# Kernel tuning notes

Measured on AMD Instinct MI355X. Metric: run time of the kernel, lower is better.

## Reference

```python
import jax, jax.numpy as jnp
import numpy as np

TAU = 2.0      # LIF membrane time constant
EPS = 1e-5     # BatchNorm eps
HEADS = 8
SCALE = 0.125
ALPHA = 4.0    # surrogate sigmoid sharpness

@jax.custom_vjp
def spike(x):
    return (x >= 0.0).astype(x.dtype)

def _spike_fwd(x):
    return spike(x), x

def _spike_bwd(x, g):
    s = jax.nn.sigmoid(ALPHA * x)
    return (g * ALPHA * s * (1.0 - s),)

spike.defvjp(_spike_fwd, _spike_bwd)

def lif(x_seq, v_th):
    # multi-step LIF, v_reset=0, hard reset; x_seq: [T, ...]
    def step(v, x):
        v = v + (x - v) / TAU
        s = spike(v - v_th)
        v = (1.0 - s) * v  # hard reset to 0
        return v, s
    v0 = jnp.zeros_like(x_seq[0])
    _, spikes = jax.lax.scan(step, v0, x_seq)
    return spikes

def bn(x, gamma, beta, mean, var):
    # inference-mode BatchNorm1d over channel axis; x: [T,B,C,N], params: [C]
    inv = gamma * jax.lax.rsqrt(var + EPS)
    return x * inv[:, None] + (beta - mean * inv)[:, None]

def setup_inputs() -> dict:
    key = jax.random.key(0)
    k1, k2 = jax.random.split(key)
    T, B, C, N, H = 4, 64, 512, 196, HEADS
    x = jax.random.normal(k1, (T, B, C, N), dtype=jnp.float32)
    res_attn = jnp.zeros((T, B, H, N, N), dtype=jnp.float32)
    w = jax.random.normal(k2, (4, C, C), dtype=jnp.float32) / np.sqrt(C)
    bn_gamma = jnp.ones((4, C), dtype=jnp.float32)
    bn_beta = jnp.zeros((4, C), dtype=jnp.float32)
    bn_mean = jnp.zeros((4, C), dtype=jnp.float32)
    bn_var = jnp.ones((4, C), dtype=jnp.float32)
    return {"x": x, "res_attn": res_attn, "w": w, "bn_gamma": bn_gamma,
            "bn_beta": bn_beta, "bn_mean": bn_mean, "bn_var": bn_var}

def reference(x, res_attn, w, bn_gamma, bn_beta, bn_mean, bn_var):
    T, B, C, N = x.shape
    H = HEADS
    D = C // H

    def qkv_branch(i):
        y = jnp.einsum('oc,tbcn->tbon', w[i], x)          # conv1x1
        y = bn(y, bn_gamma[i], bn_beta[i], bn_mean[i], bn_var[i])
        return lif(y, 1.0)                                # binary spikes

    def to_heads(t):  # [T,B,C,N] -> [T,B,H,N,D]
        return t.transpose(0, 1, 3, 2).reshape(T, B, N, H, D).transpose(0, 1, 3, 2, 4)

    q = to_heads(qkv_branch(0))
    k = to_heads(qkv_branch(1))
    v = to_heads(qkv_branch(2))

    attn = jnp.einsum('tbhnd,tbhmd->tbhnm', q, k) * SCALE
    o = jnp.einsum('tbhnm,tbhmd->tbhnd', attn, v)
    o = o.transpose(0, 1, 2, 4, 3).reshape(T, B, C, N)    # [T,B,H,D,N] -> [T,B,C,N]
    o = lif(o, 0.5)                                       # attn_lif, v_threshold=0.5
    o = jnp.einsum('oc,tbcn->tbon', w[3], o)              # proj conv1x1
    o = bn(o, bn_gamma[3], bn_beta[3], bn_mean[3], bn_var[3])
    o = lif(o, 1.0)                                       # proj_lif
    return (o, attn)
```

## Files before the change

kernel.cpp:

```cpp
#include <hip/hip_runtime.h>
#include <stdint.h>
#include <math.h>

#define T_ 4
#define B_ 64
#define C_ 512
#define N_ 196
#define H_ 8
#define OE_ 25690112ull
#define TBHN (T_*B_*H_*N_)

using u16 = unsigned short;
using u32 = unsigned int;
using u64 = unsigned long long;
using u8  = unsigned char;

typedef __attribute__((ext_vector_type(8))) short bf16x8;
typedef __attribute__((ext_vector_type(4))) float f32x4;
typedef const float __attribute__((address_space(4))) cfloat_as4;

typedef const void __attribute__((address_space(1))) gvoid;
typedef void __attribute__((address_space(3))) svoid;

__device__ __forceinline__ void gld_lds4(const void* g, void* l){
  __builtin_amdgcn_global_load_lds((gvoid*)g, (svoid*)l, 4, 0, 0);
}

__device__ __forceinline__ float b2f(u16 u){
  union { u32 i; float f; } x; x.i = ((u32)u) << 16; return x.f;
}
__device__ __forceinline__ u16 f2b(float f){
  union { float g; u32 i; } x; x.g = f; return (u16)(x.i >> 16);
}
__device__ __forceinline__ float ldf(const void* p, size_t i, bool f32){
  return f32 ? ((const float*)p)[i] : b2f(((const u16*)p)[i]);
}
__device__ __forceinline__ bool is_f32(const void* var){
  return ((const u32*)var)[0] == 0x3F800000u;
}

__global__ __launch_bounds__(256) void transpose_w(
    const void* __restrict__ w, float* __restrict__ wT, const void* __restrict__ var)
{
  const bool f32 = is_f32(var);
  __shared__ float tile[32][33];
  const int br = blockIdx.z;
  const int c0 = blockIdx.x*32, o0 = blockIdx.y*32;
  const int tx = threadIdx.x & 31, ty = threadIdx.x >> 5;
  const size_t base = (size_t)br*C_*C_;
  #pragma unroll
  for (int r = 0; r < 32; r += 8)
    tile[ty+r][tx] = ldf(w, base + (size_t)(o0+ty+r)*C_ + (c0+tx), f32);
  __syncthreads();
  #pragma unroll
  for (int r = 0; r < 32; r += 8)
    wT[base + (size_t)(c0+ty+r)*C_ + (o0+tx)] = tile[tx][ty+r];
}

template<int DT>
__device__ __forceinline__ void conv_main(
    const void* __restrict__ xin, const float* __restrict__ wp,
    u8* __restrict__ xsraw, const int wv, const int lane, const int fl0,
    float acc[4][8])
{
  const size_t cn   = (size_t)C_*N_;
  const size_t tstr = (size_t)B_*cn;

  int e0;
  if (DT == 0)      e0 = lane;
  else if (DT == 1) e0 = 2*(lane & 31);
  else              e0 = 4*(lane & 15);
  const int fl = fl0 + e0;
  const int b  = fl / N_;
  const int n  = fl - b*N_;
  const size_t lbase = (size_t)wv*tstr + (size_t)b*cn + (size_t)n;

  auto issue = [&](int k){
    const int buf = k & 1;
    const int rb  = (buf*4 + wv)*8;
    if (DT == 2){
      const u8* bp = (const u8*)xin + lbase;
      #pragma unroll
      for (int g = 0; g < 2; g++){
        const int cl = g*4 + (lane >> 4);
        gld_lds4(bp + (size_t)(k*8 + cl)*N_, xsraw + (size_t)(rb + g*4)*64);
      }
    } else if (DT == 0){
      const float* bp = (const float*)xin + lbase;
      #pragma unroll
      for (int cl = 0; cl < 8; cl++){
        gld_lds4(bp + (size_t)(k*8 + cl)*N_, xsraw + (size_t)(rb + cl)*256);
      }
    } else {
      const u16* bp = (const u16*)xin + lbase;
      #pragma unroll
      for (int p = 0; p < 4; p++){
        const int cl = p*2 + (lane >> 5);
        gld_lds4(bp + (size_t)(k*8 + cl)*N_, xsraw + (size_t)(rb + p*2)*128);
      }
    }
  };

  issue(0);
  for (int k = 0; k < 64; k++){
    __syncthreads();
    if (k + 1 < 64) issue(k + 1);
    const int buf = k & 1;
    #pragma unroll
    for (int cc = 0; cc < 8; cc++){
      const int c = (k << 3) + cc;
      float xv[4];
      #pragma unroll
      for (int t = 0; t < 4; t++){
        const int ei = ((buf*4 + t)*8 + cc)*64 + lane;
        if (DT == 2)      xv[t] = (float)xsraw[ei];
        else if (DT == 0) xv[t] = ((const float*)xsraw)[ei];
        else              xv[t] = b2f(((const u16*)xsraw)[ei]);
      }
      cfloat_as4* wr = (cfloat_as4*)(uintptr_t)(wp + (size_t)c*C_);
      #pragma unroll
      for (int j = 0; j < 8; j++){
        const float ww = wr[j];
        #pragma unroll
        for (int t = 0; t < 4; t++) acc[t][j] = fmaf(ww, xv[t], acc[t][j]);
      }
    }
  }
}

template<int IN_U8, int OUT_MODE>
__global__ __launch_bounds__(256, 4) void conv_gld(
    const void* __restrict__ xin, const float* __restrict__ wT,
    const void* __restrict__ gamma, const void* __restrict__ beta,
    const void* __restrict__ mean,  const void* __restrict__ var,
    int br, float vth, void* __restrict__ outp)
{
  __shared__ __align__(16) u8 xsraw[16384];
  __shared__ u32 P[4*64];
  const bool f32 = is_f32(var);
  const int tid  = threadIdx.x;
  const int lane = tid & 63;
  const int wv   = tid >> 6;
  const int cb   = blockIdx.y;
  const int co0  = __builtin_amdgcn_readfirstlane(cb*32 + wv*8);
  const int fl0  = blockIdx.x*64;
  const int fl   = fl0 + lane;
  const int b    = fl / N_;
  const int n    = fl - b*N_;

  if (OUT_MODE == 0){ P[tid] = 0; }

  float acc[4][8];
  #pragma unroll
  for (int t=0;t<4;t++)
    #pragma unroll
    for (int j=0;j<8;j++) acc[t][j] = 0.f;

  const float* __restrict__ wp = wT + (size_t)br*C_*C_ + co0;

  if (IN_U8)    conv_main<2>(xin, wp, xsraw, wv, lane, fl0, acc);
  else if (f32) conv_main<0>(xin, wp, xsraw, wv, lane, fl0, acc);
  else          conv_main<1>(xin, wp, xsraw, wv, lane, fl0, acc);

  {
    #pragma clang fp contract(off)
    u32 m8[4] = {0,0,0,0};
    #pragma unroll
    for (int j=0;j<8;j++){
      const int co = co0 + j;
      const size_t pb = (size_t)br*C_ + co;
      const float gf  = ldf(gamma, pb, f32);
      const float bef = ldf(beta,  pb, f32);
      const float mnf = ldf(mean,  pb, f32);
      const float vrf = ldf(var,   pb, f32);
      const float rs   = 1.0f / sqrtf(vrf + 1e-5f);
      const float invf = gf * rs;
      const float mi   = mnf * invf;
      const float shf  = bef - mi;
      float vm = 0.f;
      #pragma unroll
      for (int t=0;t<4;t++){
        float xy = acc[t][j] * invf;
        float x  = xy + shf;
        float d  = x - vm;
        float v  = vm + d * 0.5f;
        bool  s  = (v >= vth);
        vm = s ? 0.f : v;
        if (OUT_MODE == 0){
          m8[t] |= (s ? 1u : 0u) << j;
        } else {
          size_t off = ((size_t)(t*B_ + b)*C_ + co)*(size_t)N_ + n;
          if (OUT_MODE == 1){
            ((u8*)outp)[off] = s ? 1 : 0;
          } else {
            if (f32) ((float*)outp)[off] = s ? 1.f : 0.f;
            else     ((u16*)outp)[off]   = s ? (u16)0x3F80 : (u16)0;
          }
        }
      }
    }
    if (OUT_MODE == 0){
      #pragma unroll
      for (int t=0;t<4;t++)
        atomicOr(&P[t*64 + lane], m8[t] << (wv*8));
    }
  }
  if (OUT_MODE == 0){
    __syncthreads();
    const int t2 = tid >> 6, l2 = tid & 63;
    const int f2 = blockIdx.x*64 + l2;
    const int b2 = f2 / N_, n2 = f2 - b2*N_;
    const int h2 = cb >> 1, half = cb & 1;
    ((u32*)outp)[(((size_t)(t2*B_ + b2)*H_ + h2)*N_ + n2)*2 + half] = P[tid];
  }
}

__global__ __launch_bounds__(256) void attnqk_mfma(
    const u64* __restrict__ q64, const u64* __restrict__ k64,
    void* __restrict__ outp ,
    const u8* __restrict__ sv, u8* __restrict__ s3,
    const void* __restrict__ var)
{
  const bool f32 = is_f32(var);
  __shared__ __align__(16) u8  Vu[64*232];
  __shared__ __align__(16) u16 At[16*232];
  const int nt  = blockIdx.x;
  const int gy  = blockIdx.y;
  const int h   = gy & 7, b = gy >> 3;
  const int tid = threadIdx.x;
  const int lane = tid & 63;
  const int mrow = lane & 15, quad = lane >> 4;
  const int d0  = (tid >> 6) * 16;
  const int n0  = nt * 16;
  const bool wvalid = (nt < 12) || (quad == 0);
  float vmem[4] = {0.f, 0.f, 0.f, 0.f};

  for (int t = 0; t < 4; t++){
    const size_t tb  = (size_t)t*B_ + b;
    const size_t tbh = tb*H_ + h;
    __syncthreads();
    {
      const u32* vb = (const u32*)(sv + (tb*C_ + (size_t)h*64)*(size_t)N_);
      #pragma unroll
      for (int it = 0; it < 15; it++){
        int i = it*256 + tid;
        if (i < 64*58){
          int r = i / 58, wd = i - r*58;
          u32 v = (wd < 49) ? vb[r*49 + wd] : 0u;
          *(u32*)(Vu + r*232 + wd*4) = v;
        }
      }
    }
    {
      const u64* kr = k64 + tbh*(size_t)N_;
      const u64* qr = q64 + tbh*(size_t)N_;
      const size_t abase = OE_ + tbh*(size_t)(N_*N_);
      #pragma unroll
      for (int it = 0; it < 7; it++){
        int i = it*256 + tid;
        int r = i / 112, mp = i - r*112;
        int n = n0 + r;
        int m0 = mp*2;
        u64 qv = (n < N_) ? qr[n] : 0ull;
        u64 kk0 = (m0 < N_)     ? kr[m0]     : 0ull;
        u64 kk1 = (m0 + 1 < N_) ? kr[m0 + 1] : 0ull;
        float c0 = (float)__popcll(qv & kk0);
        float c1 = (float)__popcll(qv & kk1);
        *(u32*)(At + r*232 + m0) = (u32)f2b(c0) | ((u32)f2b(c1) << 16);
        if (n < N_ && m0 < N_){
          size_t e = abase + (size_t)n*N_ + m0;
          if (f32){
            float2 st; st.x = c0*0.125f; st.y = c1*0.125f;
            *(float2*)((float*)outp + e) = st;
          } else {
            *(u32*)((u16*)outp + e) =
                (u32)f2b(c0*0.125f) | ((u32)f2b(c1*0.125f) << 16);
          }
        }
      }
    }
    __syncthreads();
    f32x4 acc = {0.f, 0.f, 0.f, 0.f};
    #pragma unroll
    for (int k = 0; k < 7; k++){
      bf16x8 av = *(const bf16x8*)(At + mrow*232 + k*32 + quad*8);
      u64 vx = *(const u64*)(Vu + (d0+mrow)*232 + k*32 + quad*8);
      u32 x0 = (u32)vx, x1 = (u32)(vx >> 32);
      u32 o0 = (x0 & 1u)*0x3F80u         + (x0 & 0x100u)*0x3F8000u;
      u32 o1 = ((x0 >> 16) & 1u)*0x3F80u + ((x0 >> 16) & 0x100u)*0x3F8000u;
      u32 o2 = (x1 & 1u)*0x3F80u         + (x1 & 0x100u)*0x3F8000u;
      u32 o3 = ((x1 >> 16) & 1u)*0x3F80u + ((x1 >> 16) & 0x100u)*0x3F8000u;
      union { u32 w[4]; bf16x8 v; } bu;
      bu.w[0] = o0; bu.w[1] = o1; bu.w[2] = o2; bu.w[3] = o3;
      acc = __builtin_amdgcn_mfma_f32_16x16x32_bf16(av, bu.v, acc, 0, 0, 0);
    }
    {
      #pragma clang fp contract(off)
      u32 pk = 0;
      #pragma unroll
      for (int r = 0; r < 4; r++){
        float o  = acc[r] * 0.125f;
        float dd = o - vmem[r];
        float v  = vmem[r] + dd * 0.5f;
        bool  s  = (v >= 0.5f);
        vmem[r] = s ? 0.f : v;
        pk |= (s ? 1u : 0u) << (8*r);
      }
      if (wvalid){
        const int d = d0 + mrow;
        *(u32*)(s3 + (tb*C_ + (size_t)h*64 + d)*(size_t)N_ + n0 + quad*4) = pk;
      }
    }
  }
}

extern "C" void kernel_launch(void* const* d_in, const int* in_sizes, int n_in,
                              void* d_out, int out_size, void* d_ws, size_t ws_size,
                              hipStream_t stream)
{
  (void)in_sizes; (void)n_in; (void)out_size; (void)ws_size;
  const void* x     = d_in[0];
  const void* w     = d_in[2];
  const void* gamma = d_in[3];
  const void* beta  = d_in[4];
  const void* mean  = d_in[5];
  const void* var   = d_in[6];

  u8*  sv  = (u8*)d_ws;
  u8*  s3  = sv + OE_;
  u64* q64 = (u64*)(s3 + OE_);
  u64* k64 = q64 + TBHN;
  float* wT = (float*)(k64 + TBHN);

  transpose_w<<<dim3(16,16,4), 256, 0, stream>>>(w, wT, var);

  dim3 cgrid(196, 16);
  conv_gld<0,0><<<cgrid, 256, 0, stream>>>(x, wT, gamma, beta, mean, var, 0, 1.0f, (void*)q64);
  conv_gld<0,0><<<cgrid, 256, 0, stream>>>(x, wT, gamma, beta, mean, var, 1, 1.0f, (void*)k64);
  conv_gld<0,1><<<cgrid, 256, 0, stream>>>(x, wT, gamma, beta, mean, var, 2, 1.0f, (void*)sv);

  attnqk_mfma<<<dim3(13, B_*H_), 256, 0, stream>>>(q64, k64, d_out, sv, s3, var);

  conv_gld<1,2><<<cgrid, 256, 0, stream>>>((const void*)s3, wT, gamma, beta, mean, var, 3, 1.0f, d_out);
}
```

Before: 2.269 ms.

## Fuse Q, K and V 1x1 convolutions into one kernel sharing x loads

Replaces three separate conv launches for the Q, K and V branches with a single kernel that loads each x tile once into LDS and accumulates all three branches. Each warp now handles 4 output channels per branch instead of 8, and the grid doubles along channels. The aim is to cut the input x traffic from global memory to a third. The cost is more registers for three accumulator sets and smaller per-block channel tiles, which may raise weight-load traffic and lower occupancy. Q and K bit-packing is rewritten as 16-bit quarters per head.

```diff
diff --git a/kernel.cpp b/kernel.cpp
--- a/kernel.cpp
+++ b/kernel.cpp
@@ -58,6 +58,162 @@
 }
 
 template<int DT>
+__device__ __forceinline__ void conv_qkv_main(
+    const void* __restrict__ xin, const float* const* __restrict__ wp,
+    u8* __restrict__ xsraw, const int wv, const int lane, const int fl0,
+    float acc[3][4][4])
+{
+  const size_t cn   = (size_t)C_*N_;
+  const size_t tstr = (size_t)B_*cn;
+
+  int e0;
+  if (DT == 0) e0 = lane;
+  else         e0 = 2*(lane & 31);
+  const int fl = fl0 + e0;
+  const int b  = fl / N_;
+  const int n  = fl - b*N_;
+  const size_t lbase = (size_t)wv*tstr + (size_t)b*cn + (size_t)n;
+
+  auto issue = [&](int k){
+    const int buf = k & 1;
+    const int rb  = (buf*4 + wv)*8;
+    if (DT == 0){
+      const float* bp = (const float*)xin + lbase;
+      #pragma unroll
+      for (int cl = 0; cl < 8; cl++){
+        gld_lds4(bp + (size_t)(k*8 + cl)*N_, xsraw + (size_t)(rb + cl)*256);
+      }
+    } else {
+      const u16* bp = (const u16*)xin + lbase;
+      #pragma unroll
+      for (int p = 0; p < 4; p++){
+        const int cl = p*2 + (lane >> 5);
+        gld_lds4(bp + (size_t)(k*8 + cl)*N_, xsraw + (size_t)(rb + p*2)*128);
+      }
+    }
+  };
+
+  issue(0);
+  for (int k = 0; k < 64; k++){
+    __syncthreads();
+    if (k + 1 < 64) issue(k + 1);
+    const int buf = k & 1;
+    #pragma unroll
+    for (int cc = 0; cc < 8; cc++){
+      const int c = (k << 3) + cc;
+      float xv[4];
+      #pragma unroll
+      for (int t = 0; t < 4; t++){
+        const int ei = ((buf*4 + t)*8 + cc)*64 + lane;
+        xv[t] = (DT == 0) ? ((const float*)xsraw)[ei]
+                          : b2f(((const u16*)xsraw)[ei]);
+      }
+      #pragma unroll
+      for (int br = 0; br < 3; br++){
+        cfloat_as4* wr = (cfloat_as4*)(uintptr_t)(wp[br] + (size_t)c*C_);
+        #pragma unroll
+        for (int j = 0; j < 4; j++){
+          const float ww = wr[j];
+          #pragma unroll
+          for (int t = 0; t < 4; t++)
+            acc[br][t][j] = fmaf(ww, xv[t], acc[br][t][j]);
+        }
+      }
+    }
+  }
+}
+
+__global__ __launch_bounds__(256, 4) void conv_qkv(
+    const void* __restrict__ xin, const float* __restrict__ wT,
+    const void* __restrict__ gamma, const void* __restrict__ beta,
+    const void* __restrict__ mean,  const void* __restrict__ var,
+    u16* __restrict__ q16, u16* __restrict__ k16, u8* __restrict__ svp)
+{
+  __shared__ __align__(16) u8 xsraw[16384];
+  __shared__ u32 P[2][256];
+  const bool f32 = is_f32(var);
+  const int tid  = threadIdx.x;
+  const int lane = tid & 63;
+  const int wv   = tid >> 6;
+  const int cb   = blockIdx.y;
+  const int co0  = __builtin_amdgcn_readfirstlane(cb*16 + wv*4);
+  const int h    = cb >> 2;
+  const int quarter = cb & 3;
+  const int fl0  = blockIdx.x*64;
+  const int fl   = fl0 + lane;
+  const int b    = fl / N_;
+  const int n    = fl - b*N_;
+
+  P[0][tid] = 0; P[1][tid] = 0;
+
+  float acc[3][4][4];
+  #pragma unroll
+  for (int br=0;br<3;br++)
+    #pragma unroll
+    for (int t=0;t<4;t++)
+      #pragma unroll
+      for (int j=0;j<4;j++) acc[br][t][j] = 0.f;
+
+  const float* wp[3] = { wT + co0, wT + (size_t)C_*C_ + co0,
+                         wT + (size_t)2*C_*C_ + co0 };
+
+  if (f32) conv_qkv_main<0>(xin, wp, xsraw, wv, lane, fl0, acc);
+  else     conv_qkv_main<1>(xin, wp, xsraw, wv, lane, fl0, acc);
+
+  {
+    #pragma clang fp contract(off)
+    u32 mq[4] = {0,0,0,0}, mk[4] = {0,0,0,0};
+    #pragma unroll
+    for (int br = 0; br < 3; br++){
+      #pragma unroll
+      for (int j = 0; j < 4; j++){
+        const int co = co0 + j;
+        const size_t pb = (size_t)br*C_ + co;
+        const float gf  = ldf(gamma, pb, f32);
+        const float bef = ldf(beta,  pb, f32);
+        const float mnf = ldf(mean,  pb, f32);
+        const float vrf = ldf(var,   pb, f32);
+        const float rs   = 1.0f / sqrtf(vrf + 1e-5f);
+        const float invf = gf * rs;
+        const float mi   = mnf * invf;
+        const float shf  = bef - mi;
+        float vm = 0.f;
+        #pragma unroll
+        for (int t = 0; t < 4; t++){
+          float xy = acc[br][t][j] * invf;
+          float x  = xy + shf;
+          float d  = x - vm;
+          float v  = vm + d * 0.5f;
+          bool  s  = (v >= 1.0f);
+          vm = s ? 0.f : v;
+          if (br == 2){
+            svp[((size_t)(t*B_ + b)*C_ + co)*(size_t)N_ + n] = s ? 1 : 0;
+          } else if (br == 0){
+            mq[t] |= (s ? 1u : 0u) << j;
+          } else {
+            mk[t] |= (s ? 1u : 0u) << j;
+          }
+        }
+      }
+    }
+    #pragma unroll
+    for (int t = 0; t < 4; t++){
+      atomicOr(&P[0][t*64 + lane], mq[t] << (wv*4));
+      atomicOr(&P[1][t*64 + lane], mk[t] << (wv*4));
+    }
+  }
+  __syncthreads();
+  {
+    const int t2 = tid >> 6, l2 = tid & 63;
+    const int f2 = fl0 + l2;
+    const int b2 = f2 / N_, n2 = f2 - b2*N_;
+    const size_t idx = (((size_t)(t2*B_ + b2)*H_ + h)*(size_t)N_ + n2)*4 + quarter;
+    q16[idx] = (u16)P[0][tid];
+    k16[idx] = (u16)P[1][tid];
+  }
+}
+
+template<int DT>
 __device__ __forceinline__ void conv_main(
     const void* __restrict__ xin, const float* __restrict__ wp,
     u8* __restrict__ xsraw, const int wv, const int lane, const int fl0,
@@ -136,7 +292,6 @@
     int br, float vth, void* __restrict__ outp)
 {
   __shared__ __align__(16) u8 xsraw[16384];
-  __shared__ u32 P[4*64];
   const bool f32 = is_f32(var);
   const int tid  = threadIdx.x;
   const int lane = tid & 63;
@@ -148,8 +303,6 @@
   const int b    = fl / N_;
   const int n    = fl - b*N_;
 
-  if (OUT_MODE == 0){ P[tid] = 0; }
-
   float acc[4][8];
   #pragma unroll
   for (int t=0;t<4;t++)
@@ -164,7 +317,6 @@
 
   {
     #pragma clang fp contract(off)
-    u32 m8[4] = {0,0,0,0};
     #pragma unroll
     for (int j=0;j<8;j++){
       const int co = co0 + j;
@@ -186,32 +338,15 @@
         float v  = vm + d * 0.5f;
         bool  s  = (v >= vth);
         vm = s ? 0.f : v;
-        if (OUT_MODE == 0){
-          m8[t] |= (s ? 1u : 0u) << j;
+        size_t off = ((size_t)(t*B_ + b)*C_ + co)*(size_t)N_ + n;
+        if (OUT_MODE == 1){
+          ((u8*)outp)[off] = s ? 1 : 0;
         } else {
-          size_t off = ((size_t)(t*B_ + b)*C_ + co)*(size_t)N_ + n;
-          if (OUT_MODE == 1){
-            ((u8*)outp)[off] = s ? 1 : 0;
-          } else {
-            if (f32) ((float*)outp)[off] = s ? 1.f : 0.f;
-            else     ((u16*)outp)[off]   = s ? (u16)0x3F80 : (u16)0;
-          }
+          if (f32) ((float*)outp)[off] = s ? 1.f : 0.f;
+          else     ((u16*)outp)[off]   = s ? (u16)0x3F80 : (u16)0;
         }
       }
     }
-    if (OUT_MODE == 0){
-      #pragma unroll
-      for (int t=0;t<4;t++)
-        atomicOr(&P[t*64 + lane], m8[t] << (wv*8));
-    }
-  }
-  if (OUT_MODE == 0){
-    __syncthreads();
-    const int t2 = tid >> 6, l2 = tid & 63;
-    const int f2 = blockIdx.x*64 + l2;
-    const int b2 = f2 / N_, n2 = f2 - b2*N_;
-    const int h2 = cb >> 1, half = cb & 1;
-    ((u32*)outp)[(((size_t)(t2*B_ + b2)*H_ + h2)*N_ + n2)*2 + half] = P[tid];
   }
 }
 
@@ -334,12 +469,11 @@
 
   transpose_w<<<dim3(16,16,4), 256, 0, stream>>>(w, wT, var);
 
-  dim3 cgrid(196, 16);
-  conv_gld<0,0><<<cgrid, 256, 0, stream>>>(x, wT, gamma, beta, mean, var, 0, 1.0f, (void*)q64);
-  conv_gld<0,0><<<cgrid, 256, 0, stream>>>(x, wT, gamma, beta, mean, var, 1, 1.0f, (void*)k64);
-  conv_gld<0,1><<<cgrid, 256, 0, stream>>>(x, wT, gamma, beta, mean, var, 2, 1.0f, (void*)sv);
+  conv_qkv<<<dim3(196, 32), 256, 0, stream>>>(x, wT, gamma, beta, mean, var,
+                                              (u16*)q64, (u16*)k64, sv);
 
   attnqk_mfma<<<dim3(13, B_*H_), 256, 0, stream>>>(q64, k64, d_out, sv, s3, var);
 
-  conv_gld<1,2><<<cgrid, 256, 0, stream>>>((const void*)s3, wT, gamma, beta, mean, var, 3, 1.0f, d_out);
-}
+  conv_gld<1,2><<<dim3(196, 16), 256, 0, stream>>>((const void*)s3, wT, gamma, beta,
+                                                   mean, var, 3, 1.0f, d_out);
+}
```

Measured after the change: 2.470 ms. +8.9%, slower.

## Merge Q/K/V conv launches, reorder grid for weight reuse, deepen K-chunk to 16

Applied to the files above, without the earlier changes.

Replaces three separate Q/K/V 1x1-conv launches with one kernel whose grid z-dimension selects the branch. The grid is reordered so the output-channel block is the fastest index, letting consecutive blocks share the same input columns in cache. The input-channel chunk per pipeline stage doubles from 8 to 16, which halves the number of barriers but doubles LDS use to 32KB per block. That larger LDS footprint may reduce occupancy below the four blocks per CU the launch bounds request.

```diff
diff --git a/kernel.cpp b/kernel.cpp
--- a/kernel.cpp
+++ b/kernel.cpp
@@ -77,42 +77,42 @@
 
   auto issue = [&](int k){
     const int buf = k & 1;
-    const int rb  = (buf*4 + wv)*8;
+    const int rb  = (buf*4 + wv)*16;
     if (DT == 2){
       const u8* bp = (const u8*)xin + lbase;
       #pragma unroll
-      for (int g = 0; g < 2; g++){
+      for (int g = 0; g < 4; g++){
         const int cl = g*4 + (lane >> 4);
-        gld_lds4(bp + (size_t)(k*8 + cl)*N_, xsraw + (size_t)(rb + g*4)*64);
+        gld_lds4(bp + (size_t)(k*16 + cl)*N_, xsraw + (size_t)(rb + g*4)*64);
       }
     } else if (DT == 0){
       const float* bp = (const float*)xin + lbase;
       #pragma unroll
-      for (int cl = 0; cl < 8; cl++){
-        gld_lds4(bp + (size_t)(k*8 + cl)*N_, xsraw + (size_t)(rb + cl)*256);
+      for (int cl = 0; cl < 16; cl++){
+        gld_lds4(bp + (size_t)(k*16 + cl)*N_, xsraw + (size_t)(rb + cl)*256);
       }
     } else {
       const u16* bp = (const u16*)xin + lbase;
       #pragma unroll
-      for (int p = 0; p < 4; p++){
+      for (int p = 0; p < 8; p++){
         const int cl = p*2 + (lane >> 5);
-        gld_lds4(bp + (size_t)(k*8 + cl)*N_, xsraw + (size_t)(rb + p*2)*128);
+        gld_lds4(bp + (size_t)(k*16 + cl)*N_, xsraw + (size_t)(rb + p*2)*128);
       }
     }
   };
 
   issue(0);
-  for (int k = 0; k < 64; k++){
+  for (int k = 0; k < 32; k++){
     __syncthreads();
-    if (k + 1 < 64) issue(k + 1);
+    if (k + 1 < 32) issue(k + 1);
     const int buf = k & 1;
     #pragma unroll
-    for (int cc = 0; cc < 8; cc++){
-      const int c = (k << 3) + cc;
+    for (int cc = 0; cc < 16; cc++){
+      const int c = (k << 4) + cc;
       float xv[4];
       #pragma unroll
       for (int t = 0; t < 4; t++){
-        const int ei = ((buf*4 + t)*8 + cc)*64 + lane;
+        const int ei = ((buf*4 + t)*16 + cc)*64 + lane;
         if (DT == 2)      xv[t] = (float)xsraw[ei];
         else if (DT == 0) xv[t] = ((const float*)xsraw)[ei];
         else              xv[t] = b2f(((const u16*)xsraw)[ei]);
@@ -128,27 +128,27 @@
   }
 }
 
-template<int IN_U8, int OUT_MODE>
-__global__ __launch_bounds__(256, 4) void conv_gld(
+__global__ __launch_bounds__(256, 4) void conv_qkv(
     const void* __restrict__ xin, const float* __restrict__ wT,
     const void* __restrict__ gamma, const void* __restrict__ beta,
     const void* __restrict__ mean,  const void* __restrict__ var,
-    int br, float vth, void* __restrict__ outp)
-{
-  __shared__ __align__(16) u8 xsraw[16384];
-  __shared__ u32 P[4*64];
+    u32* __restrict__ q32, u32* __restrict__ k32, u8* __restrict__ svp)
+{
+  __shared__ __align__(16) u8 xsraw[32768];
+  __shared__ u32 P[256];
   const bool f32 = is_f32(var);
   const int tid  = threadIdx.x;
   const int lane = tid & 63;
   const int wv   = tid >> 6;
-  const int cb   = blockIdx.y;
+  const int cb   = blockIdx.x;
+  const int br   = blockIdx.z;
   const int co0  = __builtin_amdgcn_readfirstlane(cb*32 + wv*8);
-  const int fl0  = blockIdx.x*64;
+  const int fl0  = blockIdx.y*64;
   const int fl   = fl0 + lane;
   const int b    = fl / N_;
   const int n    = fl - b*N_;
 
-  if (OUT_MODE == 0){ P[tid] = 0; }
+  if (br < 2){ P[tid] = 0; }
 
   float acc[4][8];
   #pragma unroll
@@ -158,9 +158,8 @@
 
   const float* __restrict__ wp = wT + (size_t)br*C_*C_ + co0;
 
-  if (IN_U8)    conv_main<2>(xin, wp, xsraw, wv, lane, fl0, acc);
-  else if (f32) conv_main<0>(xin, wp, xsraw, wv, lane, fl0, acc);
-  else          conv_main<1>(xin, wp, xsraw, wv, lane, fl0, acc);
+  if (f32) conv_main<0>(xin, wp, xsraw, wv, lane, fl0, acc);
+  else     conv_main<1>(xin, wp, xsraw, wv, lane, fl0, acc);
 
   {
     #pragma clang fp contract(off)
@@ -184,34 +183,88 @@
         float x  = xy + shf;
         float d  = x - vm;
         float v  = vm + d * 0.5f;
-        bool  s  = (v >= vth);
+        bool  s  = (v >= 1.0f);
         vm = s ? 0.f : v;
-        if (OUT_MODE == 0){
+        if (br == 2){
+          svp[((size_t)(t*B_ + b)*C_ + co)*(size_t)N_ + n] = s ? 1 : 0;
+        } else {
           m8[t] |= (s ? 1u : 0u) << j;
-        } else {
-          size_t off = ((size_t)(t*B_ + b)*C_ + co)*(size_t)N_ + n;
-          if (OUT_MODE == 1){
-            ((u8*)outp)[off] = s ? 1 : 0;
-          } else {
-            if (f32) ((float*)outp)[off] = s ? 1.f : 0.f;
-            else     ((u16*)outp)[off]   = s ? (u16)0x3F80 : (u16)0;
-          }
         }
       }
     }
-    if (OUT_MODE == 0){
+    if (br < 2){
       #pragma unroll
       for (int t=0;t<4;t++)
         atomicOr(&P[t*64 + lane], m8[t] << (wv*8));
     }
   }
-  if (OUT_MODE == 0){
+  if (br < 2){
     __syncthreads();
     const int t2 = tid >> 6, l2 = tid & 63;
-    const int f2 = blockIdx.x*64 + l2;
+    const int f2 = fl0 + l2;
     const int b2 = f2 / N_, n2 = f2 - b2*N_;
     const int h2 = cb >> 1, half = cb & 1;
-    ((u32*)outp)[(((size_t)(t2*B_ + b2)*H_ + h2)*N_ + n2)*2 + half] = P[tid];
+    u32* dst = (br == 0) ? q32 : k32;
+    dst[(((size_t)(t2*B_ + b2)*H_ + h2)*(size_t)N_ + n2)*2 + half] = P[tid];
+  }
+}
+
+__global__ __launch_bounds__(256, 4) void conv_proj(
+    const void* __restrict__ xin, const float* __restrict__ wT,
+    const void* __restrict__ gamma, const void* __restrict__ beta,
+    const void* __restrict__ mean,  const void* __restrict__ var,
+    void* __restrict__ outp)
+{
+  __shared__ __align__(16) u8 xsraw[32768];
+  const bool f32 = is_f32(var);
+  const int tid  = threadIdx.x;
+  const int lane = tid & 63;
+  const int wv   = tid >> 6;
+  const int cb   = blockIdx.x;
+  const int co0  = __builtin_amdgcn_readfirstlane(cb*32 + wv*8);
+  const int fl0  = blockIdx.y*64;
+  const int fl   = fl0 + lane;
+  const int b    = fl / N_;
+  const int n    = fl - b*N_;
+
+  float acc[4][8];
+  #pragma unroll
+  for (int t=0;t<4;t++)
+    #pragma unroll
+    for (int j=0;j<8;j++) acc[t][j] = 0.f;
+
+  const float* __restrict__ wp = wT + (size_t)3*C_*C_ + co0;
+
+  conv_main<2>(xin, wp, xsraw, wv, lane, fl0, acc);
+
+  {
+    #pragma clang fp contract(off)
+    #pragma unroll
+    for (int j=0;j<8;j++){
+      const int co = co0 + j;
+      const size_t pb = (size_t)3*C_ + co;
+      const float gf  = ldf(gamma, pb, f32);
+      const float bef = ldf(beta,  pb, f32);
+      const float mnf = ldf(mean,  pb, f32);
+      const float vrf = ldf(var,   pb, f32);
+      const float rs   = 1.0f / sqrtf(vrf + 1e-5f);
+      const float invf = gf * rs;
+      const float mi   = mnf * invf;
+      const float shf  = bef - mi;
+      float vm = 0.f;
+      #pragma unroll
+      for (int t=0;t<4;t++){
+        float xy = acc[t][j] * invf;
+        float x  = xy + shf;
+        float d  = x - vm;
+        float v  = vm + d * 0.5f;
+        bool  s  = (v >= 1.0f);
+        vm = s ? 0.f : v;
+        size_t off = ((size_t)(t*B_ + b)*C_ + co)*(size_t)N_ + n;
+        if (f32) ((float*)outp)[off] = s ? 1.f : 0.f;
+        else     ((u16*)outp)[off]   = s ? (u16)0x3F80 : (u16)0;
+      }
+    }
   }
 }
 
@@ -334,12 +387,11 @@
 
   transpose_w<<<dim3(16,16,4), 256, 0, stream>>>(w, wT, var);
 
-  dim3 cgrid(196, 16);
-  conv_gld<0,0><<<cgrid, 256, 0, stream>>>(x, wT, gamma, beta, mean, var, 0, 1.0f, (void*)q64);
-  conv_gld<0,0><<<cgrid, 256, 0, stream>>>(x, wT, gamma, beta, mean, var, 1, 1.0f, (void*)k64);
-  conv_gld<0,1><<<cgrid, 256, 0, stream>>>(x, wT, gamma, beta, mean, var, 2, 1.0f, (void*)sv);
+  conv_qkv<<<dim3(16, 196, 3), 256, 0, stream>>>(x, wT, gamma, beta, mean, var,
+                                                 (u32*)q64, (u32*)k64, sv);
 
   attnqk_mfma<<<dim3(13, B_*H_), 256, 0, stream>>>(q64, k64, d_out, sv, s3, var);
 
-  conv_gld<1,2><<<cgrid, 256, 0, stream>>>((const void*)s3, wT, gamma, beta, mean, var, 3, 1.0f, d_out);
-}
+  conv_proj<<<dim3(16, 196), 256, 0, stream>>>((const void*)s3, wT, gamma, beta,
+                                               mean, var, d_out);
+}
```

After: 2.342 ms. 1.03x slower.
